# Kernel tuning notes

Hardware: AMD Instinct MI355X
Metric: run time of the kernel (lower is better)

## Reference

```python
import jax, jax.numpy as jnp
import numpy as np

K_SIZE = 5
PAD = 2  # (dilation*(k-1)+1 - stride + 1)//2 with k=5, dilation=1, stride=1
DEPTH_MAX = 192.0
SAMPLE_NUM = 15


def setup_inputs() -> dict:
    key = jax.random.key(0)
    k1, k2, k3, k4 = jax.random.split(key, 4)
    b, c, h, w = 2, 32, 256, 512
    depth = jax.random.uniform(k1, (b, 1, h, w), jnp.float32) * 100.0
    features = jax.random.normal(k2, (b, c, h, w), jnp.float32)
    guide_weight = jax.random.uniform(k3, (b, h, w, K_SIZE * K_SIZE), jnp.float32)
    sample_idx = jax.random.randint(k4, (SAMPLE_NUM,), 0, K_SIZE * K_SIZE, dtype=jnp.int32)
    return {"depth": depth, "features": features, "guide_weight": guide_weight,
            "sample_idx": sample_idx}


def _gather(xpad, rows, cols):
    # xpad [b,c,H+2p,W+2p]; rows [s,h], cols [s,w] -> [b,c,s,h,w]
    return xpad[:, :, rows[:, :, None], cols[:, None, :]]


def reference(depth, features, guide_weight, sample_idx):
    b, c, h, w = features.shape
    d = depth.reshape(b, h, w)
    valid = ((d > 0) & (d < DEPTH_MAX)).astype(features.dtype)[:, None]  # [b,1,h,w]

    # Gaussian positional weights of the sampled kernel offsets (select_index)
    ctr = K_SIZE // 2
    px = (sample_idx % K_SIZE).astype(jnp.float32)
    py = (sample_idx // K_SIZE).astype(jnp.float32)
    dis = jnp.sqrt((px - ctr) ** 2 + (py - ctr) ** 2)
    pos_w = jnp.exp(-0.5 * dis)
    pos_w = pos_w / jnp.sum(pos_w)  # [s]

    # Direct gather at sampled kernel offsets (equivalent to unfold + index_select).
    # torch Unfold kernel-position ordering is row-major: p -> (ky=p//K, kx=p%K).
    dy = sample_idx // K_SIZE
    dx = sample_idx % K_SIZE
    rows = dy[:, None] + jnp.arange(h)[None, :]  # [s,h] indices into padded image
    cols = dx[:, None] + jnp.arange(w)[None, :]  # [s,w]

    fpad = jnp.pad(features, ((0, 0), (0, 0), (PAD, PAD), (PAD, PAD)))
    vpad = jnp.pad(valid, ((0, 0), (0, 0), (PAD, PAD), (PAD, PAD)))

    sampled = _gather(fpad, rows, cols)            # [b,c,s,h,w]
    valid_s = _gather(vpad, rows, cols)[:, 0]      # [b,s,h,w]
    guide_s = jnp.take(guide_weight, sample_idx, axis=3)    # [b,h,w,s]
    guide_s = jnp.transpose(guide_s, (0, 3, 1, 2))          # [b,s,h,w]

    wgt = valid_s * pos_w[None, :, None, None] * guide_s    # use_position & use_guide
    wgt = jax.nn.softmax(wgt, axis=1)
    out = jnp.einsum('bcshw,bshw->bchw', sampled, wgt)
    return (out, features)
```

## Files before the change

### kernel.cpp

```cpp
#include <hip/hip_runtime.h>
#include <math.h>

#define K_SIZE 5
#define PAD 2
#define DEPTH_MAX 192.0f
#define S_NUM 15
#define G_NUM (K_SIZE * K_SIZE)

#define B_DIM 2
#define C_DIM 32
#define H_DIM 256
#define W_DIM 512
#define HW (H_DIM * W_DIM)
#define NPX (B_DIM * HW)

#define TX 256
#define CH_PER 16
#define LROW 272
#define LDS_F (5 * LROW)
#define NGRP (5 * 68)
#define CTR_IDX (2 * LROW + 4)
#define WREG 1020

__global__ __launch_bounds__(256) void adaptive_fused_v11(
    const float* __restrict__ depth,
    const float* __restrict__ features,
    const float* __restrict__ guide,
    const int*   __restrict__ sample_idx,
    float*       __restrict__ out)
{
    __shared__ float lds_raw[3 * LDS_F];
    float (*sbuf)[LDS_F] = reinterpret_cast<float (*)[LDS_F]>(lds_raw);

    const int t    = threadIdx.x;
    const int lane = t & 63;
    const int wv   = t >> 6;

    const int orig = blockIdx.x;
    const int lid  = (orig & 7) * 128 + (orig >> 3);
    const int tile = lid & 1;
    const int y    = (lid >> 1) & (H_DIM - 1);
    const int b    = lid >> 9;
    const int x0   = tile * TX;
    const int x    = x0 + t;
    const int c0   = blockIdx.y * CH_PER;

    int sidx[S_NUM];
#pragma unroll
    for (int s = 0; s < S_NUM; ++s) sidx[s] = sample_idx[s];

    int soff0, soff1 = 0;
    int lidx0, lidx1 = 0;
    {
        const int g   = t;
        const int row = g / 68;
        const int col = (g - row * 68) * 4;
        lidx0 = row * LROW + col;
        int ir = y + row - 2; ir = ir < 0 ? 0 : (ir > H_DIM - 1 ? H_DIM - 1 : ir);
        int ic = x0 - 4 + col; ic = ic < 0 ? 0 : (ic > W_DIM - 4 ? W_DIM - 4 : ic);
        soff0 = ir * W_DIM + ic;
    }
    const bool has2 = (t < NGRP - 256);
    if (has2) {
        const int g   = 256 + t;
        const int row = g / 68;
        const int col = (g - row * 68) * 4;
        lidx1 = row * LROW + col;
        int ir = y + row - 2; ir = ir < 0 ? 0 : (ir > H_DIM - 1 ? H_DIM - 1 : ir);
        int ic = x0 - 4 + col; ic = ic < 0 ? 0 : (ic > W_DIM - 4 ? W_DIM - 4 : ic);
        soff1 = ir * W_DIM + ic;
    }

    const size_t hw  = (size_t)HW;
    const float* fpl = features + ((size_t)b * C_DIM + c0) * hw;

    float4 a0, a1, r0, r1;
    a0 = *(const float4*)(fpl + soff0);
    if (has2) a1 = *(const float4*)(fpl + soff1);
    {
        const float* f1 = fpl + hw;
        r0 = *(const float4*)(f1 + soff0);
        if (has2) r1 = *(const float4*)(f1 + soff1);
    }

    float posw[S_NUM];
    float psum = 0.f;
#pragma unroll
    for (int s = 0; s < S_NUM; ++s) {
        const float px = (float)(sidx[s] % K_SIZE);
        const float py = (float)(sidx[s] / K_SIZE);
        const float ddx = px - (float)(K_SIZE / 2);
        const float ddy = py - (float)(K_SIZE / 2);
        posw[s] = expf(-0.5f * sqrtf(ddx * ddx + ddy * ddy));
        psum += posw[s];
    }
    const float inv_psum = 1.f / psum;

    float pv[S_NUM];
    unsigned inbm = 0;
    const int dbase = b * HW;
#pragma unroll
    for (int s = 0; s < S_NUM; ++s) {
        const int dy = sidx[s] / K_SIZE - PAD;
        const int dx = sidx[s] % K_SIZE - PAD;
        const int yy = y + dy;
        const int xx = x + dx;
        const bool inb = (yy >= 0) & (yy < H_DIM) & (xx >= 0) & (xx < W_DIM);
        float v = 0.f;
        if (inb) {
            const float d = depth[dbase + yy * W_DIM + xx];
            v = (d > 0.f && d < DEPTH_MAX) ? 1.f : 0.f;
        }
        pv[s] = v * (posw[s] * inv_psum);
        inbm |= (unsigned)inb << s;
    }

    float raw[S_NUM];
    {
        float* wreg = &lds_raw[wv * WREG];
        const float* gbase =
            guide + (size_t)(b * HW + y * W_DIM + x0 + wv * 64) * G_NUM;
        {
            const float4* gsrc = (const float4*)gbase;
            float4* gdst = (float4*)wreg;
#pragma unroll
            for (int k = 0; k < 4; ++k) {
                const int idx = k * 64 + lane;
                if (idx < 200) gdst[idx] = gsrc[idx];
            }
        }
        __builtin_amdgcn_wave_barrier();
        if (lane < 32) {
            const float* gr = &wreg[lane * G_NUM];
#pragma unroll
            for (int s = 0; s < S_NUM; ++s) raw[s] = pv[s] * gr[sidx[s]];
        }
        __builtin_amdgcn_wave_barrier();
        {
            const float4* gsrc = (const float4*)(gbase + 32 * G_NUM);
            float4* gdst = (float4*)wreg;
#pragma unroll
            for (int k = 0; k < 4; ++k) {
                const int idx = k * 64 + lane;
                if (idx < 200) gdst[idx] = gsrc[idx];
            }
        }
        __builtin_amdgcn_wave_barrier();
        if (lane >= 32) {
            const float* gr = &wreg[(lane - 32) * G_NUM];
#pragma unroll
            for (int s = 0; s < S_NUM; ++s) raw[s] = pv[s] * gr[sidx[s]];
        }
    }

    float mx = raw[0];
#pragma unroll
    for (int s = 1; s < S_NUM; ++s) mx = fmaxf(mx, raw[s]);
    float esum = 0.f;
    float wgt[S_NUM];
#pragma unroll
    for (int s = 0; s < S_NUM; ++s) {
        wgt[s] = expf(raw[s] - mx);
        esum += wgt[s];
    }
    const float inv_esum = 1.f / esum;
#pragma unroll
    for (int s = 0; s < S_NUM; ++s)
        wgt[s] = wgt[s] * inv_esum * (((inbm >> s) & 1u) ? 1.f : 0.f);

    int ldsoff[S_NUM];
#pragma unroll
    for (int s = 0; s < S_NUM; ++s) {
        const int si = sidx[s];
        ldsoff[s] = (si / K_SIZE) * LROW + t + (si % K_SIZE) + 2;
    }

    __syncthreads();

    *(float4*)&sbuf[0][lidx0] = a0;
    if (has2) *(float4*)&sbuf[0][lidx1] = a1;
    __syncthreads();

    float* o0 = out + ((size_t)b * C_DIM + c0) * hw + (size_t)y * W_DIM + x0 + t;
    float* o1 = o0 + (size_t)B_DIM * C_DIM * hw;

#pragma unroll
    for (int c = 0; c < CH_PER; ++c) {
        if (c + 1 < CH_PER) {
            float* dst = sbuf[(c + 1) % 3];
            *(float4*)&dst[lidx0] = r0;
            if (has2) *(float4*)&dst[lidx1] = r1;
        }
        float4 t0, t1;
        if (c + 2 < CH_PER) {
            const float* fn = fpl + (size_t)(c + 2) * hw;
            t0 = *(const float4*)(fn + soff0);
            if (has2) t1 = *(const float4*)(fn + soff1);
        }

        const float* src = sbuf[c % 3];
        float acc = 0.f;
#pragma unroll
        for (int s = 0; s < S_NUM; ++s)
            acc = fmaf(src[ldsoff[s]], wgt[s], acc);
        const float ctr = src[CTR_IDX + t];

        o0[(size_t)c * hw] = acc;
        o1[(size_t)c * hw] = ctr;

        if (c + 2 < CH_PER) { r0 = t0; if (has2) r1 = t1; }
        __syncthreads();
    }
}

extern "C" void kernel_launch(void* const* d_in, const int* in_sizes, int n_in,
                              void* d_out, int out_size, void* d_ws, size_t ws_size,
                              hipStream_t stream) {
    const float* depth      = (const float*)d_in[0];
    const float* features   = (const float*)d_in[1];
    const float* guide      = (const float*)d_in[2];
    const int*   sample_idx = (const int*)d_in[3];

    float* out = (float*)d_out;
    dim3 grid(NPX / TX, C_DIM / CH_PER, 1);

    adaptive_fused_v11<<<grid, 256, 0, stream>>>(depth, features, guide,
                                                 sample_idx, out);
}
```

Baseline: 144.8 us.

## Process all channels per block in interleaved pairs, dropping channel-split grid

```diff
diff --git a/kernel.cpp b/kernel.cpp
--- a/kernel.cpp
+++ b/kernel.cpp
@@ -15,22 +15,23 @@
 #define NPX (B_DIM * HW)
 
 #define TX 256
-#define CH_PER 16
 #define LROW 272
 #define LDS_F (5 * LROW)
+#define PAIR_F (2 * LDS_F)
 #define NGRP (5 * 68)
 #define CTR_IDX (2 * LROW + 4)
+#define NPAIR 16
 #define WREG 1020
 
-__global__ __launch_bounds__(256) void adaptive_fused_v11(
+__global__ __launch_bounds__(256, 4) void adaptive_fused_v12(
     const float* __restrict__ depth,
     const float* __restrict__ features,
     const float* __restrict__ guide,
     const int*   __restrict__ sample_idx,
     float*       __restrict__ out)
 {
-    __shared__ float lds_raw[3 * LDS_F];
-    float (*sbuf)[LDS_F] = reinterpret_cast<float (*)[LDS_F]>(lds_raw);
+    __shared__ float lds_raw[3 * PAIR_F];
+    float (*sbuf)[PAIR_F] = reinterpret_cast<float (*)[PAIR_F]>(lds_raw);
 
     const int t    = threadIdx.x;
     const int lane = t & 63;
@@ -43,19 +44,16 @@
     const int b    = lid >> 9;
     const int x0   = tile * TX;
     const int x    = x0 + t;
-    const int c0   = blockIdx.y * CH_PER;
 
     int sidx[S_NUM];
 #pragma unroll
     for (int s = 0; s < S_NUM; ++s) sidx[s] = sample_idx[s];
 
     int soff0, soff1 = 0;
-    int lidx0, lidx1 = 0;
     {
         const int g   = t;
         const int row = g / 68;
         const int col = (g - row * 68) * 4;
-        lidx0 = row * LROW + col;
         int ir = y + row - 2; ir = ir < 0 ? 0 : (ir > H_DIM - 1 ? H_DIM - 1 : ir);
         int ic = x0 - 4 + col; ic = ic < 0 ? 0 : (ic > W_DIM - 4 ? W_DIM - 4 : ic);
         soff0 = ir * W_DIM + ic;
@@ -65,22 +63,30 @@
         const int g   = 256 + t;
         const int row = g / 68;
         const int col = (g - row * 68) * 4;
-        lidx1 = row * LROW + col;
         int ir = y + row - 2; ir = ir < 0 ? 0 : (ir > H_DIM - 1 ? H_DIM - 1 : ir);
         int ic = x0 - 4 + col; ic = ic < 0 ? 0 : (ic > W_DIM - 4 ? W_DIM - 4 : ic);
         soff1 = ir * W_DIM + ic;
     }
 
     const size_t hw  = (size_t)HW;
-    const float* fpl = features + ((size_t)b * C_DIM + c0) * hw;
-
-    float4 a0, a1, r0, r1;
-    a0 = *(const float4*)(fpl + soff0);
-    if (has2) a1 = *(const float4*)(fpl + soff1);
-    {
-        const float* f1 = fpl + hw;
-        r0 = *(const float4*)(f1 + soff0);
-        if (has2) r1 = *(const float4*)(f1 + soff1);
+    const float* fpl = features + (size_t)b * C_DIM * hw;
+
+    float4 aA0, aB0, aA1, aB1;
+    float4 rA0, rB0, rA1, rB1;
+    aA0 = *(const float4*)(fpl + soff0);
+    aB0 = *(const float4*)(fpl + hw + soff0);
+    if (has2) {
+        aA1 = *(const float4*)(fpl + soff1);
+        aB1 = *(const float4*)(fpl + hw + soff1);
+    }
+    {
+        const float* f2 = fpl + 2 * hw;
+        rA0 = *(const float4*)(f2 + soff0);
+        rB0 = *(const float4*)(f2 + hw + soff0);
+        if (has2) {
+            rA1 = *(const float4*)(f2 + soff1);
+            rB1 = *(const float4*)(f2 + hw + soff1);
+        }
     }
 
     float posw[S_NUM];
@@ -177,38 +183,71 @@
 
     __syncthreads();
 
-    *(float4*)&sbuf[0][lidx0] = a0;
-    if (has2) *(float4*)&sbuf[0][lidx1] = a1;
+    {
+        float* dst = sbuf[0];
+        float4 w0, w1;
+        w0.x = aA0.x; w0.y = aB0.x; w0.z = aA0.y; w0.w = aB0.y;
+        w1.x = aA0.z; w1.y = aB0.z; w1.z = aA0.w; w1.w = aB0.w;
+        *(float4*)&dst[8 * t]     = w0;
+        *(float4*)&dst[8 * t + 4] = w1;
+        if (has2) {
+            w0.x = aA1.x; w0.y = aB1.x; w0.z = aA1.y; w0.w = aB1.y;
+            w1.x = aA1.z; w1.y = aB1.z; w1.z = aA1.w; w1.w = aB1.w;
+            *(float4*)&dst[8 * (256 + t)]     = w0;
+            *(float4*)&dst[8 * (256 + t) + 4] = w1;
+        }
+    }
     __syncthreads();
 
-    float* o0 = out + ((size_t)b * C_DIM + c0) * hw + (size_t)y * W_DIM + x0 + t;
+    float* o0 = out + (size_t)b * C_DIM * hw + (size_t)y * W_DIM + x0 + t;
     float* o1 = o0 + (size_t)B_DIM * C_DIM * hw;
 
 #pragma unroll
-    for (int c = 0; c < CH_PER; ++c) {
-        if (c + 1 < CH_PER) {
-            float* dst = sbuf[(c + 1) % 3];
-            *(float4*)&dst[lidx0] = r0;
-            if (has2) *(float4*)&dst[lidx1] = r1;
-        }
-        float4 t0, t1;
-        if (c + 2 < CH_PER) {
-            const float* fn = fpl + (size_t)(c + 2) * hw;
-            t0 = *(const float4*)(fn + soff0);
-            if (has2) t1 = *(const float4*)(fn + soff1);
-        }
-
-        const float* src = sbuf[c % 3];
-        float acc = 0.f;
-#pragma unroll
-        for (int s = 0; s < S_NUM; ++s)
-            acc = fmaf(src[ldsoff[s]], wgt[s], acc);
-        const float ctr = src[CTR_IDX + t];
-
-        o0[(size_t)c * hw] = acc;
-        o1[(size_t)c * hw] = ctr;
-
-        if (c + 2 < CH_PER) { r0 = t0; if (has2) r1 = t1; }
+    for (int p = 0; p < NPAIR; ++p) {
+        if (p + 1 < NPAIR) {
+            float* dst = sbuf[(p + 1) % 3];
+            float4 w0, w1;
+            w0.x = rA0.x; w0.y = rB0.x; w0.z = rA0.y; w0.w = rB0.y;
+            w1.x = rA0.z; w1.y = rB0.z; w1.z = rA0.w; w1.w = rB0.w;
+            *(float4*)&dst[8 * t]     = w0;
+            *(float4*)&dst[8 * t + 4] = w1;
+            if (has2) {
+                w0.x = rA1.x; w0.y = rB1.x; w0.z = rA1.y; w0.w = rB1.y;
+                w1.x = rA1.z; w1.y = rB1.z; w1.z = rA1.w; w1.w = rB1.w;
+                *(float4*)&dst[8 * (256 + t)]     = w0;
+                *(float4*)&dst[8 * (256 + t) + 4] = w1;
+            }
+        }
+        float4 nA0, nB0, nA1, nB1;
+        if (p + 2 < NPAIR) {
+            const float* fn = fpl + (size_t)(2 * (p + 2)) * hw;
+            nA0 = *(const float4*)(fn + soff0);
+            nB0 = *(const float4*)(fn + hw + soff0);
+            if (has2) {
+                nA1 = *(const float4*)(fn + soff1);
+                nB1 = *(const float4*)(fn + hw + soff1);
+            }
+        }
+
+        const float* src = sbuf[p % 3];
+        float accA = 0.f, accB = 0.f;
+#pragma unroll
+        for (int s = 0; s < S_NUM; ++s) {
+            const float2 v = *(const float2*)&src[2 * ldsoff[s]];
+            accA = fmaf(v.x, wgt[s], accA);
+            accB = fmaf(v.y, wgt[s], accB);
+        }
+        const float2 ctr = *(const float2*)&src[2 * (CTR_IDX + t)];
+
+        o0[(size_t)(2 * p) * hw]     = accA;
+        o0[(size_t)(2 * p + 1) * hw] = accB;
+        o1[(size_t)(2 * p) * hw]     = ctr.x;
+        o1[(size_t)(2 * p + 1) * hw] = ctr.y;
+
+        if (p + 2 < NPAIR) {
+            rA0 = nA0; rB0 = nB0;
+            if (has2) { rA1 = nA1; rB1 = nB1; }
+        }
         __syncthreads();
     }
 }
@@ -222,8 +261,8 @@
     const int*   sample_idx = (const int*)d_in[3];
 
     float* out = (float*)d_out;
-    dim3 grid(NPX / TX, C_DIM / CH_PER, 1);
-
-    adaptive_fused_v11<<<grid, 256, 0, stream>>>(depth, features, guide,
-                                                 sample_idx, out);
+    const int blocks = NPX / TX;
+
+    adaptive_fused_v12<<<blocks, 256, 0, stream>>>(depth, features, guide,
+                                                   sample_idx, out);
 }
```

After: 134.3 us, median of 2. -7.3%, faster.
